# Kernel tuning notes

Measured on AMD Instinct MI355X. Metric: run time of the kernel, lower is better.

## Reference

```python
import jax, jax.numpy as jnp
import numpy as np

N_DST = 50000


def setup_inputs() -> dict:
    key = jax.random.key(0)
    k1, k2, k3, k4, k5, k6 = jax.random.split(key, 6)
    n_src, n_dst, n_edges, d_in, d_out = 50000, 50000, 1600000, 128, 128
    return {
        "h_neigh": jax.random.normal(k1, (n_src, d_in), dtype=jnp.float32),
        "h_self": jax.random.normal(k2, (n_dst, d_in), dtype=jnp.float32),
        "src_idx": jax.random.randint(k3, (n_edges,), 0, n_src, dtype=jnp.int32),
        "dst_idx": jax.random.randint(k4, (n_edges,), 0, n_dst, dtype=jnp.int32),
        "W_self": jax.random.normal(k5, (d_out, d_in), dtype=jnp.float32) * 0.05,
        "W_neigh": jax.random.normal(k6, (d_out, d_in), dtype=jnp.float32) * 0.05,
    }


def reference(h_neigh, h_self, src_idx, dst_idx, W_self, W_neigh):
    # mean aggregation over edges: for each dst node, mean of src features
    msgs = h_neigh[src_idx]                                   # [E, d_in]
    summed = jax.ops.segment_sum(msgs, dst_idx, num_segments=N_DST)  # [N_dst, d_in]
    deg = jax.ops.segment_sum(jnp.ones_like(dst_idx, dtype=h_neigh.dtype),
                              dst_idx, num_segments=N_DST)    # [N_dst]
    agg = summed / jnp.maximum(deg, 1.0)[:, None]             # mean; 0 for isolated nodes

    z = h_self @ W_self.T + agg @ W_neigh.T                   # [N_dst, d_out]
    z = jax.nn.relu(z)
    # L2 normalize rows, guarding zero norms
    z_norm = jnp.linalg.norm(z, axis=1, keepdims=True)
    z_norm = jnp.where(z_norm == 0, 1.0, z_norm)
    return z / z_norm
```

## Files before the change

kernel.cpp:

```cpp
#include <hip/hip_runtime.h>
#include <hip/hip_bf16.h>

#define DFEAT 128
#define BSH 7
#define CAP 4608

typedef short short8 __attribute__((ext_vector_type(8)));
typedef unsigned short ushort8 __attribute__((ext_vector_type(8)));
typedef float f32x4 __attribute__((ext_vector_type(4)));

__global__ void prep_kernel(const float2* __restrict__ in, __hip_bfloat162* __restrict__ out,
                            int n2, int nconv, int n_src,
                            const float* __restrict__ Wself, const float* __restrict__ Wneigh,
                            unsigned short* __restrict__ wcat, int* __restrict__ gcursor) {
    int b = blockIdx.x;
    int tid = threadIdx.x;
    if (b < nconv) {
        int i = b * 256 + tid;
        if (i < n2) {
            float2 v = in[i];
            __hip_bfloat162 o;
            o.x = __float2bfloat16(v.x);
            o.y = __float2bfloat16(v.y);
            out[i] = o;
        }
    } else {
        int bb = b - nconv;
        int idx = bb * 256 + tid;
        int j = idx >> 8, k = idx & 255;
        float v = (k < DFEAT) ? Wself[j * DFEAT + k] : Wneigh[j * DFEAT + k - DFEAT];
        __hip_bfloat16 h = __float2bfloat16(v);
        wcat[idx] = *(unsigned short*)&h;
        if (bb < 2) {
            int s = bb * 256 + tid;
            gcursor[s] = s * CAP;
        }
        if (bb == 2 && tid < DFEAT) {
            ((unsigned short*)out)[(size_t)n_src * DFEAT + tid] = 0;
        }
    }
}

__global__ void partition_kernel(const int* __restrict__ src, const int* __restrict__ dst,
                                 int E, int* __restrict__ gcursor,
                                 unsigned* __restrict__ pairs) {
    __shared__ int hist[512];
    __shared__ int base[512];
    int tid = threadIdx.x;
    for (int b0 = blockIdx.x * 2048; b0 < E; b0 += gridDim.x * 2048) {
        hist[tid] = 0;
        hist[tid + 256] = 0;
        __syncthreads();
        int eb = b0 + tid * 8;
        int ss[8], dd[8];
        if (eb + 8 <= E) {
            int4 s0 = *(const int4*)(src + eb);
            int4 s1 = *(const int4*)(src + eb + 4);
            int4 d0 = *(const int4*)(dst + eb);
            int4 d1 = *(const int4*)(dst + eb + 4);
            ss[0] = s0.x; ss[1] = s0.y; ss[2] = s0.z; ss[3] = s0.w;
            ss[4] = s1.x; ss[5] = s1.y; ss[6] = s1.z; ss[7] = s1.w;
            dd[0] = d0.x; dd[1] = d0.y; dd[2] = d0.z; dd[3] = d0.w;
            dd[4] = d1.x; dd[5] = d1.y; dd[6] = d1.z; dd[7] = d1.w;
        } else {
#pragma unroll
            for (int e = 0; e < 8; ++e) {
                int i = eb + e;
                ss[e] = (i < E) ? src[i] : 0;
                dd[e] = (i < E) ? dst[i] : -1;
            }
        }
        unsigned mypk[8];
        int mybin[8], myrank[8];
#pragma unroll
        for (int e = 0; e < 8; ++e) {
            mybin[e] = -1;
            if (eb + e < E) {
                unsigned d = (unsigned)dd[e];
                int bin = d >> BSH;
                mybin[e] = bin;
                myrank[e] = atomicAdd(&hist[bin], 1);
                mypk[e] = (d << 16) | (unsigned)ss[e];
            }
        }
        __syncthreads();
        if (hist[tid]) base[tid] = atomicAdd(&gcursor[tid], hist[tid]);
        if (hist[tid + 256]) base[tid + 256] = atomicAdd(&gcursor[tid + 256], hist[tid + 256]);
        __syncthreads();
#pragma unroll
        for (int e = 0; e < 8; ++e)
            if (mybin[e] >= 0) pairs[base[mybin[e]] + myrank[e]] = mypk[e];
        __syncthreads();
    }
}

__global__ void fine_fill_kernel(const unsigned* __restrict__ pairs,
                                 const int* __restrict__ gcursor,
                                 int* __restrict__ row_start, int* __restrict__ deg,
                                 unsigned short* __restrict__ csr16, int n_dst) {
    __shared__ int hist[256];
    __shared__ int cur[256];
    __shared__ int wtot[4];
    int b = blockIdx.x;
    int tid = threadIdx.x;
    int lo = b * CAP, hi = gcursor[b];
    hist[tid] = 0;
    __syncthreads();
    for (int j = lo + tid; j < hi; j += 256)
        atomicAdd(&hist[(pairs[j] >> 16) & 127], 1);
    __syncthreads();
    int v = hist[tid];
    int lane = tid & 63, w = tid >> 6;
    int x = v;
    for (int off = 1; off < 64; off <<= 1) {
        int t = __shfl_up(x, off);
        if (lane >= off) x += t;
    }
    if (lane == 63) wtot[w] = x;
    __syncthreads();
    if (tid == 0) {
        int r = 0;
        for (int i = 0; i < 4; ++i) { int t = wtot[i]; wtot[i] = r; r += t; }
    }
    __syncthreads();
    int excl = x + wtot[w] - v;
    cur[tid] = excl;
    int d = (b << BSH) + tid;
    if (tid < (1 << BSH) && d < n_dst) {
        row_start[d] = lo + excl;
        deg[d] = v;
    }
    __syncthreads();
    for (int j = lo + tid; j < hi; j += 256) {
        unsigned p = pairs[j];
        int slot = atomicAdd(&cur[(p >> 16) & 127], 1);
        csr16[lo + slot] = (unsigned short)(p & 0xFFFFu);
    }
}

template <int PASS>
__global__ void aggregate_kernel(const unsigned short* __restrict__ hnb,
                                 const unsigned short* __restrict__ csr16,
                                 const int* __restrict__ row_start,
                                 const int* __restrict__ deg,
                                 unsigned short* __restrict__ agb, int n_dst, int zrow) {
    int gtid = blockIdx.x * blockDim.x + threadIdx.x;
    int d = gtid >> 6;
    if (d >= n_dst) return;
    int lane = threadIdx.x & 63;
    int beg = row_start[d];
    int dg = deg[d];
    int slot = lane >> 3;
    int fl = lane & 7;
    const unsigned short* tab = hnb + PASS * 64 + fl * 8;
    float a[8] = {0.f, 0.f, 0.f, 0.f, 0.f, 0.f, 0.f, 0.f};
    for (int base = 0; base < dg; base += 64) {
        int s = (base + lane < dg) ? (int)csr16[beg + base + lane] : zrow;
        int lim = dg - base;
        if (lim > 64) lim = 64;
        for (int j = 0; j < lim; j += 32) {
            int i0 = __shfl(s, j + slot);
            int i1 = __shfl(s, j + 8 + slot);
            int i2 = __shfl(s, j + 16 + slot);
            int i3 = __shfl(s, j + 24 + slot);
            ushort8 v0 = *(const ushort8*)(tab + (size_t)i0 * DFEAT);
            ushort8 v1 = *(const ushort8*)(tab + (size_t)i1 * DFEAT);
            ushort8 v2 = *(const ushort8*)(tab + (size_t)i2 * DFEAT);
            ushort8 v3 = *(const ushort8*)(tab + (size_t)i3 * DFEAT);
#pragma unroll
            for (int k = 0; k < 8; ++k) a[k] += __uint_as_float((unsigned)v0[k] << 16);
#pragma unroll
            for (int k = 0; k < 8; ++k) a[k] += __uint_as_float((unsigned)v1[k] << 16);
#pragma unroll
            for (int k = 0; k < 8; ++k) a[k] += __uint_as_float((unsigned)v2[k] << 16);
#pragma unroll
            for (int k = 0; k < 8; ++k) a[k] += __uint_as_float((unsigned)v3[k] << 16);
        }
    }
#pragma unroll
    for (int k = 0; k < 8; ++k) {
        a[k] += __shfl_xor(a[k], 8);
        a[k] += __shfl_xor(a[k], 16);
        a[k] += __shfl_xor(a[k], 32);
    }
    if (lane < 8) {
        float inv = 1.0f / (float)(dg > 1 ? dg : 1);
        ushort8 o;
#pragma unroll
        for (int k = 0; k < 8; ++k) {
            __hip_bfloat16 h = __float2bfloat16(a[k] * inv);
            o[k] = *(unsigned short*)&h;
        }
        *(ushort8*)(agb + (size_t)d * DFEAT + PASS * 64 + lane * 8) = o;
    }
}

__launch_bounds__(512, 4)
__global__ void gemm_mfma_kernel(const float* __restrict__ h_self,
                                 const unsigned short* __restrict__ agb,
                                 const unsigned short* __restrict__ Wcat,
                                 float* __restrict__ out, int M) {
    __shared__ char Ws[64 * 1024];
    int tid = threadIdx.x;
    int row0 = blockIdx.x * 128;
    {
        int j = tid >> 2, q = tid & 3;
#pragma unroll
        for (int u = 0; u < 8; ++u) {
            int ks = q * 64 + u * 8;
            uint4 vv = *(const uint4*)(Wcat + j * 256 + ks);
            *(uint4*)(Ws + ((j * 512 + ks * 2) ^ ((j & 7) << 4))) = vv;
        }
    }
    __syncthreads();

    int lane = tid & 63, w = tid >> 6;
    int arow = row0 + w * 16 + (lane & 15);
    int kgrp = (lane >> 4) * 8;
    bool rv = arow < M;
    int ar = rv ? arow : 0;

    f32x4 acc[8] = {};
#pragma unroll
    for (int kstep = 0; kstep < 8; ++kstep) {
        int kk = kstep * 32 + kgrp;
        short8 a;
        if (kk < DFEAT) {
            float4 f0 = *(const float4*)(h_self + (size_t)ar * DFEAT + kk);
            float4 f1 = *(const float4*)(h_self + (size_t)ar * DFEAT + kk + 4);
            __hip_bfloat16 b0 = __float2bfloat16(f0.x), b1 = __float2bfloat16(f0.y);
            __hip_bfloat16 b2 = __float2bfloat16(f0.z), b3 = __float2bfloat16(f0.w);
            __hip_bfloat16 b4 = __float2bfloat16(f1.x), b5 = __float2bfloat16(f1.y);
            __hip_bfloat16 b6 = __float2bfloat16(f1.z), b7 = __float2bfloat16(f1.w);
            a[0] = *(short*)&b0; a[1] = *(short*)&b1; a[2] = *(short*)&b2; a[3] = *(short*)&b3;
            a[4] = *(short*)&b4; a[5] = *(short*)&b5; a[6] = *(short*)&b6; a[7] = *(short*)&b7;
        } else {
            a = *(const short8*)(agb + (size_t)ar * DFEAT + (kk - DFEAT));
        }
#pragma unroll
        for (int n = 0; n < 8; ++n) {
            int nr = n * 16 + (lane & 15);
            short8 bfrag = *(const short8*)(Ws + ((nr * 512 + kk * 2) ^ ((nr & 7) << 4)));
            acc[n] = __builtin_amdgcn_mfma_f32_16x16x32_bf16(a, bfrag, acc[n], 0, 0, 0);
        }
    }

    float ss[4] = {0.f, 0.f, 0.f, 0.f};
#pragma unroll
    for (int n = 0; n < 8; ++n)
#pragma unroll
        for (int i = 0; i < 4; ++i) {
            float z = fmaxf(acc[n][i], 0.f);
            acc[n][i] = z;
            ss[i] += z * z;
        }
#pragma unroll
    for (int i = 0; i < 4; ++i)
        for (int m = 1; m < 16; m <<= 1) ss[i] += __shfl_xor(ss[i], m);
#pragma unroll
    for (int i = 0; i < 4; ++i) {
        int grow = row0 + w * 16 + (lane >> 4) * 4 + i;
        if (grow < M) {
            float nv = sqrtf(ss[i]);
            float inv = (nv == 0.f) ? 1.f : 1.f / nv;
#pragma unroll
            for (int n = 0; n < 8; ++n)
                out[(size_t)grow * DFEAT + n * 16 + (lane & 15)] = acc[n][i] * inv;
        }
    }
}

extern "C" void kernel_launch(void* const* d_in, const int* in_sizes, int n_in,
                              void* d_out, int out_size, void* d_ws, size_t ws_size,
                              hipStream_t stream) {
    const float* h_neigh = (const float*)d_in[0];
    const float* h_self  = (const float*)d_in[1];
    const int*   src_idx = (const int*)d_in[2];
    const int*   dst_idx = (const int*)d_in[3];
    const float* W_self  = (const float*)d_in[4];
    const float* W_neigh = (const float*)d_in[5];
    float* out = (float*)d_out;

    const int D = DFEAT;
    int n_src = in_sizes[0] / D;
    int n_dst = in_sizes[1] / D;
    int E = in_sizes[2];
    int NB = (n_dst + (1 << BSH) - 1) >> BSH;

    char* wsp = (char*)d_ws;
    size_t off = 0;
    auto alloc = [&](size_t bytes) -> void* {
        void* p = wsp + off;
        off += (bytes + 255) & ~(size_t)255;
        return p;
    };
    int* gcursor          = (int*)alloc(512 * 4);
    int* row_start        = (int*)alloc((size_t)n_dst * 4);
    int* deg              = (int*)alloc((size_t)n_dst * 4);
    unsigned* pairs       = (unsigned*)alloc((size_t)NB * CAP * 4);
    unsigned short* csr16 = (unsigned short*)alloc((size_t)NB * CAP * 2 + 256);
    unsigned short* hnb   = (unsigned short*)alloc((size_t)(n_src + 1) * D * 2);
    unsigned short* agb   = (unsigned short*)alloc((size_t)n_dst * D * 2);
    unsigned short* wcat  = (unsigned short*)alloc((size_t)DFEAT * 256 * 2);
    (void)ws_size;

    int n2 = n_src * (D / 2);
    int nconv = (n2 + 255) / 256;
    prep_kernel<<<nconv + 128, 256, 0, stream>>>(
        (const float2*)h_neigh, (__hip_bfloat162*)hnb, n2, nconv, n_src,
        W_self, W_neigh, wcat, gcursor);

    partition_kernel<<<256, 256, 0, stream>>>(src_idx, dst_idx, E, gcursor, pairs);

    fine_fill_kernel<<<NB, 256, 0, stream>>>(pairs, gcursor, row_start, deg, csr16, n_dst);

    int agg_blocks = (n_dst * 64 + 255) / 256;
    aggregate_kernel<0><<<agg_blocks, 256, 0, stream>>>(hnb, csr16, row_start, deg, agb, n_dst, n_src);
    aggregate_kernel<1><<<agg_blocks, 256, 0, stream>>>(hnb, csr16, row_start, deg, agb, n_dst, n_src);

    gemm_mfma_kernel<<<(n_dst + 127) / 128, 512, 0, stream>>>(
        h_self, agb, wcat, out, n_dst);
}
```

Baseline: 114.3 us.

## Fuse edge partitioning with bf16 conversion into one kernel, add 8-edge tail loop

Merges the prep kernel (feature/weight conversion to bf16) and the partition kernel into a single launch whose first blocks partition edges and whose remaining blocks do the conversions. The global cursors become relative counts zeroed by a memset, so the partition no longer waits on the prep kernel to initialise them. The aggregation loop also gains an 8-edge remainder loop so partial groups of 32 no longer load padded rows. This removes one launch and its serialisation gap, and lets the memory-bound conversion overlap with the atomic-heavy partition, at the cost of an added memset call.

```diff
diff --git a/kernel.cpp b/kernel.cpp
--- a/kernel.cpp
+++ b/kernel.cpp
@@ -4,93 +4,91 @@
 #define DFEAT 128
 #define BSH 7
 #define CAP 4608
+#define PART_BLOCKS 256
 
 typedef short short8 __attribute__((ext_vector_type(8)));
 typedef unsigned short ushort8 __attribute__((ext_vector_type(8)));
 typedef float f32x4 __attribute__((ext_vector_type(4)));
 
-__global__ void prep_kernel(const float2* __restrict__ in, __hip_bfloat162* __restrict__ out,
-                            int n2, int nconv, int n_src,
-                            const float* __restrict__ Wself, const float* __restrict__ Wneigh,
-                            unsigned short* __restrict__ wcat, int* __restrict__ gcursor) {
-    int b = blockIdx.x;
+__global__ void fused_prep_partition_kernel(
+        const int* __restrict__ src, const int* __restrict__ dst, int E,
+        int* __restrict__ gcursor, unsigned* __restrict__ pairs,
+        const float2* __restrict__ in, __hip_bfloat162* __restrict__ out,
+        int n2, int nconv, int n_src,
+        const float* __restrict__ Wself, const float* __restrict__ Wneigh,
+        unsigned short* __restrict__ wcat) {
     int tid = threadIdx.x;
-    if (b < nconv) {
-        int i = b * 256 + tid;
-        if (i < n2) {
-            float2 v = in[i];
-            __hip_bfloat162 o;
-            o.x = __float2bfloat16(v.x);
-            o.y = __float2bfloat16(v.y);
-            out[i] = o;
+    if (blockIdx.x < PART_BLOCKS) {
+        __shared__ int hist[512];
+        __shared__ int base[512];
+        for (int b0 = blockIdx.x * 2048; b0 < E; b0 += PART_BLOCKS * 2048) {
+            hist[tid] = 0;
+            hist[tid + 256] = 0;
+            __syncthreads();
+            int eb = b0 + tid * 8;
+            int ss[8], dd[8];
+            if (eb + 8 <= E) {
+                int4 s0 = *(const int4*)(src + eb);
+                int4 s1 = *(const int4*)(src + eb + 4);
+                int4 d0 = *(const int4*)(dst + eb);
+                int4 d1 = *(const int4*)(dst + eb + 4);
+                ss[0] = s0.x; ss[1] = s0.y; ss[2] = s0.z; ss[3] = s0.w;
+                ss[4] = s1.x; ss[5] = s1.y; ss[6] = s1.z; ss[7] = s1.w;
+                dd[0] = d0.x; dd[1] = d0.y; dd[2] = d0.z; dd[3] = d0.w;
+                dd[4] = d1.x; dd[5] = d1.y; dd[6] = d1.z; dd[7] = d1.w;
+            } else {
+#pragma unroll
+                for (int e = 0; e < 8; ++e) {
+                    int i = eb + e;
+                    ss[e] = (i < E) ? src[i] : 0;
+                    dd[e] = (i < E) ? dst[i] : -1;
+                }
+            }
+            unsigned mypk[8];
+            int mybin[8], myrank[8];
+#pragma unroll
+            for (int e = 0; e < 8; ++e) {
+                mybin[e] = -1;
+                if (eb + e < E) {
+                    unsigned d = (unsigned)dd[e];
+                    int bin = d >> BSH;
+                    mybin[e] = bin;
+                    myrank[e] = atomicAdd(&hist[bin], 1);
+                    mypk[e] = (d << 16) | (unsigned)ss[e];
+                }
+            }
+            __syncthreads();
+            if (hist[tid]) base[tid] = atomicAdd(&gcursor[tid], hist[tid]);
+            if (hist[tid + 256]) base[tid + 256] = atomicAdd(&gcursor[tid + 256], hist[tid + 256]);
+            __syncthreads();
+#pragma unroll
+            for (int e = 0; e < 8; ++e)
+                if (mybin[e] >= 0)
+                    pairs[mybin[e] * CAP + base[mybin[e]] + myrank[e]] = mypk[e];
+            __syncthreads();
         }
     } else {
-        int bb = b - nconv;
-        int idx = bb * 256 + tid;
-        int j = idx >> 8, k = idx & 255;
-        float v = (k < DFEAT) ? Wself[j * DFEAT + k] : Wneigh[j * DFEAT + k - DFEAT];
-        __hip_bfloat16 h = __float2bfloat16(v);
-        wcat[idx] = *(unsigned short*)&h;
-        if (bb < 2) {
-            int s = bb * 256 + tid;
-            gcursor[s] = s * CAP;
-        }
-        if (bb == 2 && tid < DFEAT) {
-            ((unsigned short*)out)[(size_t)n_src * DFEAT + tid] = 0;
-        }
-    }
-}
-
-__global__ void partition_kernel(const int* __restrict__ src, const int* __restrict__ dst,
-                                 int E, int* __restrict__ gcursor,
-                                 unsigned* __restrict__ pairs) {
-    __shared__ int hist[512];
-    __shared__ int base[512];
-    int tid = threadIdx.x;
-    for (int b0 = blockIdx.x * 2048; b0 < E; b0 += gridDim.x * 2048) {
-        hist[tid] = 0;
-        hist[tid + 256] = 0;
-        __syncthreads();
-        int eb = b0 + tid * 8;
-        int ss[8], dd[8];
-        if (eb + 8 <= E) {
-            int4 s0 = *(const int4*)(src + eb);
-            int4 s1 = *(const int4*)(src + eb + 4);
-            int4 d0 = *(const int4*)(dst + eb);
-            int4 d1 = *(const int4*)(dst + eb + 4);
-            ss[0] = s0.x; ss[1] = s0.y; ss[2] = s0.z; ss[3] = s0.w;
-            ss[4] = s1.x; ss[5] = s1.y; ss[6] = s1.z; ss[7] = s1.w;
-            dd[0] = d0.x; dd[1] = d0.y; dd[2] = d0.z; dd[3] = d0.w;
-            dd[4] = d1.x; dd[5] = d1.y; dd[6] = d1.z; dd[7] = d1.w;
+        int pb = blockIdx.x - PART_BLOCKS;
+        if (pb < nconv) {
+            int i = pb * 256 + tid;
+            if (i < n2) {
+                float2 v = in[i];
+                __hip_bfloat162 o;
+                o.x = __float2bfloat16(v.x);
+                o.y = __float2bfloat16(v.y);
+                out[i] = o;
+            }
         } else {
-#pragma unroll
-            for (int e = 0; e < 8; ++e) {
-                int i = eb + e;
-                ss[e] = (i < E) ? src[i] : 0;
-                dd[e] = (i < E) ? dst[i] : -1;
+            int bb = pb - nconv;
+            int idx = bb * 256 + tid;
+            int j = idx >> 8, k = idx & 255;
+            float v = (k < DFEAT) ? Wself[j * DFEAT + k] : Wneigh[j * DFEAT + k - DFEAT];
+            __hip_bfloat16 h = __float2bfloat16(v);
+            wcat[idx] = *(unsigned short*)&h;
+            if (bb == 2 && tid < DFEAT) {
+                ((unsigned short*)out)[(size_t)n_src * DFEAT + tid] = 0;
             }
         }
-        unsigned mypk[8];
-        int mybin[8], myrank[8];
-#pragma unroll
-        for (int e = 0; e < 8; ++e) {
-            mybin[e] = -1;
-            if (eb + e < E) {
-                unsigned d = (unsigned)dd[e];
-                int bin = d >> BSH;
-                mybin[e] = bin;
-                myrank[e] = atomicAdd(&hist[bin], 1);
-                mypk[e] = (d << 16) | (unsigned)ss[e];
-            }
-        }
-        __syncthreads();
-        if (hist[tid]) base[tid] = atomicAdd(&gcursor[tid], hist[tid]);
-        if (hist[tid + 256]) base[tid + 256] = atomicAdd(&gcursor[tid + 256], hist[tid + 256]);
-        __syncthreads();
-#pragma unroll
-        for (int e = 0; e < 8; ++e)
-            if (mybin[e] >= 0) pairs[base[mybin[e]] + myrank[e]] = mypk[e];
-        __syncthreads();
     }
 }
 
@@ -103,7 +101,7 @@
     __shared__ int wtot[4];
     int b = blockIdx.x;
     int tid = threadIdx.x;
-    int lo = b * CAP, hi = gcursor[b];
+    int lo = b * CAP, hi = lo + gcursor[b];
     hist[tid] = 0;
     __syncthreads();
     for (int j = lo + tid; j < hi; j += 256)
@@ -158,7 +156,8 @@
         int s = (base + lane < dg) ? (int)csr16[beg + base + lane] : zrow;
         int lim = dg - base;
         if (lim > 64) lim = 64;
-        for (int j = 0; j < lim; j += 32) {
+        int j = 0;
+        for (; j + 32 <= lim; j += 32) {
             int i0 = __shfl(s, j + slot);
             int i1 = __shfl(s, j + 8 + slot);
             int i2 = __shfl(s, j + 16 + slot);
@@ -175,6 +174,12 @@
             for (int k = 0; k < 8; ++k) a[k] += __uint_as_float((unsigned)v2[k] << 16);
 #pragma unroll
             for (int k = 0; k < 8; ++k) a[k] += __uint_as_float((unsigned)v3[k] << 16);
+        }
+        for (; j < lim; j += 8) {
+            int i0 = __shfl(s, j + slot);
+            ushort8 v0 = *(const ushort8*)(tab + (size_t)i0 * DFEAT);
+#pragma unroll
+            for (int k = 0; k < 8; ++k) a[k] += __uint_as_float((unsigned)v0[k] << 16);
         }
     }
 #pragma unroll
@@ -304,13 +309,14 @@
     unsigned short* wcat  = (unsigned short*)alloc((size_t)DFEAT * 256 * 2);
     (void)ws_size;
 
+    hipMemsetAsync(gcursor, 0, 512 * 4, stream);
+
     int n2 = n_src * (D / 2);
     int nconv = (n2 + 255) / 256;
-    prep_kernel<<<nconv + 128, 256, 0, stream>>>(
+    fused_prep_partition_kernel<<<PART_BLOCKS + nconv + 128, 256, 0, stream>>>(
+        src_idx, dst_idx, E, gcursor, pairs,
         (const float2*)h_neigh, (__hip_bfloat162*)hnb, n2, nconv, n_src,
-        W_self, W_neigh, wcat, gcursor);
-
-    partition_kernel<<<256, 256, 0, stream>>>(src_idx, dst_idx, E, gcursor, pairs);
+        W_self, W_neigh, wcat);
 
     fine_fill_kernel<<<NB, 256, 0, stream>>>(pairs, gcursor, row_start, deg, csr16, n_dst);
 
```

Result: no change. 114.2 us (-0.1%).
